# Performance work log

Hardware: AMD Instinct MI355X
Metric: run time of the kernel (lower is better)

## Reference

```python
import jax, jax.numpy as jnp
import numpy as np


def setup_inputs() -> dict:
    key = jax.random.key(0)
    ks = jax.random.split(key, 7)
    B, F, D = 1024, 32, 64
    H = [128, 128, 128]
    x = jax.random.normal(ks[0], (B, F, D), dtype=jnp.float32)
    # Conv1d(k=1) weights: (out, in) where in = prev_field * F, Kaiming-ish scale
    W0 = jax.random.normal(ks[1], (H[0], F * F), dtype=jnp.float32) * 0.02
    b0 = jnp.zeros((H[0],), dtype=jnp.float32)
    W1 = jax.random.normal(ks[2], (H[1], H[0] * F), dtype=jnp.float32) * 0.02
    b1 = jnp.zeros((H[1],), dtype=jnp.float32)
    W2 = jax.random.normal(ks[3], (H[2], H[1] * F), dtype=jnp.float32) * 0.02
    b2 = jnp.zeros((H[2],), dtype=jnp.float32)
    return {"x": x, "W0": W0, "b0": b0, "W1": W1, "b1": b1, "W2": W2, "b2": b2}


def reference(x, W0, b0, W1, b1, W2, b2):
    # CIN: per layer, outer product of current hidden with base fields along
    # embed dim, then 1x1 conv (channel mix) + ReLU. We fuse the bhmd
    # intermediate directly into the contraction: W reshaped to (o, h, m)
    # matches torch's reshape(b, h*m, d) channel ordering (h major, m minor).
    F = x.shape[1]
    x0 = x  # (b, m=F, d)
    h = x
    res = []
    for W, b in ((W0, b0), (W1, b1), (W2, b2)):
        o = W.shape[0]
        Wr = W.reshape(o, h.shape[1], F)  # (o, h, m)
        z = jnp.einsum('bhd,bmd,ohm->bod', h, x0, Wr) + b[None, :, None]
        h = jax.nn.relu(z)
        res.append(h)
    out = jnp.concatenate(res, axis=1)  # (b, sum(H), d)
    return jnp.sum(out, axis=-1)  # (b, sum(H))
```

## Files before the change

### kernel.cpp

```cpp
#include <hip/hip_runtime.h>
#include <stdint.h>


typedef __attribute__((ext_vector_type(8))) _Float16 f16x8;
typedef __attribute__((ext_vector_type(2))) _Float16 f16x2;
typedef __attribute__((ext_vector_type(4))) float f32x4;
typedef __attribute__((ext_vector_type(16))) float f32x16;
typedef __attribute__((ext_vector_type(4))) int i32x4;
typedef __attribute__((ext_vector_type(2))) int i32x2;

union AB {
  i32x4 i;
  f16x8 h;
  uint32_t u[4];
};
union AB2 {
  i32x2 i;
  uint32_t u[2];
};

static __device__ __forceinline__ uint32_t pkmul(uint32_t a, uint32_t b) {
  f16x2 r = __builtin_bit_cast(f16x2, a) * __builtin_bit_cast(f16x2, b);
  return __builtin_bit_cast(uint32_t, r);
}
static __device__ __forceinline__ uint32_t pkcvt(float a, float b) {
  return __builtin_bit_cast(uint32_t, __builtin_amdgcn_cvt_pkrtz(a, b));
}

#define HP 140

__global__ __launch_bounds__(256, 4) void cin_main(
    const float* __restrict__ x, const uint16_t* __restrict__ wp,
    const float* __restrict__ bias0, const float* __restrict__ bias1,
    const float* __restrict__ bias2, float* __restrict__ out) {
  __shared__ __align__(16) uint16_t hT[64][HP];

  const int tid = threadIdx.x;
  const int ot = tid >> 6, lane = tid & 63;
  const int hi = lane >> 5;
  const int l31 = lane & 31;
  const int b = blockIdx.x;

  for (int e = tid; e < 2048; e += 256) {
    int m = e >> 6, d = e & 63;
    hT[d][m] =
        __builtin_bit_cast(uint16_t, (_Float16)x[(size_t)b * 2048 + m * 64 + d]);
  }
  __syncthreads();

  AB xf[2][2];
#pragma unroll
  for (int dt = 0; dt < 2; ++dt)
#pragma unroll
    for (int s = 0; s < 2; ++s) {
      AB2 lo = *(const AB2*)&hT[dt * 32 + l31][s * 16 + hi * 8];
      AB2 hi4 = *(const AB2*)&hT[dt * 32 + l31][s * 16 + hi * 8 + 4];
      xf[dt][s].u[0] = lo.u[0];
      xf[dt][s].u[1] = lo.u[1];
      xf[dt][s].u[2] = hi4.u[0];
      xf[dt][s].u[3] = hi4.u[1];
    }

  f32x16 acc[2][2];

#pragma unroll
  for (int L = 0; L < 3; ++L) {
    const int Kch = (L == 0) ? 32 : 128;
    const uint16_t* wl = (L == 0) ? wp : (L == 1) ? wp + 131072 : wp + 655360;
    const float* bias = (L == 0) ? bias0 : (L == 1) ? bias1 : bias2;

    const uint16_t* wptr = wl + (size_t)ot * Kch * 1024 + lane * 8;

#pragma unroll
    for (int dt = 0; dt < 2; ++dt)
#pragma unroll
      for (int s = 0; s < 2; ++s)
#pragma unroll
        for (int r = 0; r < 16; ++r) acc[dt][s][r] = 0.f;

    AB wbuf[2][4];
    uint32_t hvA[2], hvB[2];

    auto loadSlot = [&](int sl, int c) {
      int cw = (c < Kch) ? c : 0;
#pragma unroll
      for (int cc = 0; cc < 2; ++cc)
#pragma unroll
        for (int s = 0; s < 2; ++s)
          wbuf[sl][cc * 2 + s].i =
              *(const i32x4*)(wptr + (size_t)(cw + cc) * 1024 + s * 512);
    };
    auto loadHv = [&](uint32_t (&hv)[2], int c) {
      int cw = (c < Kch) ? c : 0;
#pragma unroll
      for (int dt = 0; dt < 2; ++dt)
        hv[dt] = *(const uint32_t*)&hT[dt * 32 + l31][cw];
    };
    auto computeStep = [&](const AB (&wb)[4], const uint32_t (&hv)[2]) {
#pragma unroll
      for (int cc = 0; cc < 2; ++cc) {
        uint32_t hd0 = __builtin_amdgcn_perm(hv[0], hv[0],
                                             cc ? 0x03020302u : 0x01000100u);
        uint32_t hd1 = __builtin_amdgcn_perm(hv[1], hv[1],
                                             cc ? 0x03020302u : 0x01000100u);
#pragma unroll
        for (int s = 0; s < 2; ++s) {
          AB bf0, bf1;
#pragma unroll
          for (int k = 0; k < 4; ++k) {
            bf0.u[k] = pkmul(hd0, xf[0][s].u[k]);
            bf1.u[k] = pkmul(hd1, xf[1][s].u[k]);
          }
          acc[0][s] = __builtin_amdgcn_mfma_f32_32x32x16_f16(
              wb[cc * 2 + s].h, bf0.h, acc[0][s], 0, 0, 0);
          acc[1][s] = __builtin_amdgcn_mfma_f32_32x32x16_f16(
              wb[cc * 2 + s].h, bf1.h, acc[1][s], 0, 0, 0);
        }
      }
    };

    loadSlot(0, 0);
    loadSlot(1, 2);
    loadHv(hvA, 0);

#pragma unroll 1
    for (int c0 = 0; c0 < Kch; c0 += 4) {
      loadHv(hvB, c0 + 2);
      computeStep(wbuf[0], hvA);
      loadSlot(0, c0 + 4);
      __builtin_amdgcn_sched_barrier(0);
      loadHv(hvA, c0 + 4);
      computeStep(wbuf[1], hvB);
      loadSlot(1, c0 + 6);
      __builtin_amdgcn_sched_barrier(0);
    }

    f32x16 a0, a1;
#pragma unroll
    for (int r = 0; r < 16; ++r) {
      a0[r] = acc[0][0][r] + acc[0][1][r];
      a1[r] = acc[1][0][r] + acc[1][1][r];
    }

    f32x4 bv[4];
#pragma unroll
    for (int rg = 0; rg < 4; ++rg)
      bv[rg] = *(const f32x4*)(bias + ot * 32 + 8 * rg + 4 * hi);
#pragma unroll
    for (int r = 0; r < 16; ++r) {
      a0[r] = fmaxf(a0[r] + bv[r >> 2][r & 3], 0.f);
      a1[r] = fmaxf(a1[r] + bv[r >> 2][r & 3], 0.f);
    }

    if (L < 2) {
      __syncthreads();
#pragma unroll
      for (int rg = 0; rg < 4; ++rg) {
        uint2 pk0, pk1;
        pk0.x = pkcvt(a0[4 * rg + 0], a0[4 * rg + 1]);
        pk0.y = pkcvt(a0[4 * rg + 2], a0[4 * rg + 3]);
        pk1.x = pkcvt(a1[4 * rg + 0], a1[4 * rg + 1]);
        pk1.y = pkcvt(a1[4 * rg + 2], a1[4 * rg + 3]);
        int ch = ot * 32 + 8 * rg + 4 * hi;
        *(uint2*)&hT[l31][ch] = pk0;
        *(uint2*)&hT[32 + l31][ch] = pk1;
      }
    }

#pragma unroll
    for (int rg = 0; rg < 4; ++rg) {
      f32x4 s4;
#pragma unroll
      for (int rr = 0; rr < 4; ++rr) {
        float s = a0[4 * rg + rr] + a1[4 * rg + rr];
        s += __shfl_xor(s, 1);
        s += __shfl_xor(s, 2);
        s += __shfl_xor(s, 4);
        s += __shfl_xor(s, 8);
        s += __shfl_xor(s, 16);
        s4[rr] = s;
      }
      if (l31 == 0)
        *(f32x4*)(out + (size_t)b * 384 + L * 128 + ot * 32 + 8 * rg + 4 * hi) = s4;
    }

    if (L < 2) __syncthreads();
  }
}

__global__ void pack_w_all(const float* __restrict__ W0, const float* __restrict__ W1,
                           const float* __restrict__ W2, uint16_t* __restrict__ Wp) {
  int blk = blockIdx.x;
  const float* W;
  uint16_t* dst;
  int kshift;
  if (blk < 64)       { W = W0; dst = Wp;          kshift = 5; }
  else if (blk < 320) { W = W1; dst = Wp + 131072; kshift = 7; blk -= 64; }
  else                { W = W2; dst = Wp + 655360; kshift = 7; blk -= 320; }
  int idx = blk * 256 + threadIdx.x;
  int Kq = 1 << (kshift + 2);
  int o = idx >> (kshift + 2);
  int kq = idx & (Kq - 1);
  int c = kq >> 2, s = (kq >> 1) & 1, hi = kq & 1;
  int ot = o >> 5, li = o & 31;
  const float* src = W + ((size_t)o << (kshift + 5)) + kq * 8;
  uint4 val;
  val.x = pkcvt(src[0], src[1]);
  val.y = pkcvt(src[2], src[3]);
  val.z = pkcvt(src[4], src[5]);
  val.w = pkcvt(src[6], src[7]);
  size_t d16 = ((((size_t)(ot << kshift) + c) * 2 + s) << 9) + (hi << 8) + (li << 3);
  *(uint4*)(dst + d16) = val;
}

extern "C" void kernel_launch(void* const* d_in, const int* in_sizes, int n_in,
                              void* d_out, int out_size, void* d_ws, size_t ws_size,
                              hipStream_t stream) {
  (void)in_sizes; (void)n_in; (void)out_size; (void)ws_size;
  const float* x  = (const float*)d_in[0];
  const float* W0 = (const float*)d_in[1];
  const float* b0 = (const float*)d_in[2];
  const float* W1 = (const float*)d_in[3];
  const float* b1 = (const float*)d_in[4];
  const float* W2 = (const float*)d_in[5];
  const float* b2 = (const float*)d_in[6];
  uint16_t* wpacked = (uint16_t*)d_ws;

  hipLaunchKernelGGL(pack_w_all, dim3(576), dim3(256), 0, stream, W0, W1, W2, wpacked);
  hipLaunchKernelGGL(cin_main, dim3(1024), dim3(256), 0, stream,
                     x, wpacked, b0, b1, b2, (float*)d_out);
}
```

Measured before the change: 221.7 us.

## Process two batch rows per block to reuse weight fragments across samples

Each block now handles two batch samples, so every weight fragment loaded from global memory feeds twice as many MFMAs. The grid halves, shared memory doubles and the occupancy hint drops from 4 to 3 waves per SIMD. The loop is peeled so the last step no longer issues clamped prefetches, and the weight base address is made wave-uniform through readfirstlane. This trades higher register and LDS use, and less parallelism, for lower weight-load traffic per sample.

```diff
diff --git a/kernel.cpp b/kernel.cpp
--- a/kernel.cpp
+++ b/kernel.cpp
@@ -29,37 +29,40 @@
 
 #define HP 140
 
-__global__ __launch_bounds__(256, 4) void cin_main(
+__global__ __launch_bounds__(256, 3) void cin_main(
     const float* __restrict__ x, const uint16_t* __restrict__ wp,
     const float* __restrict__ bias0, const float* __restrict__ bias1,
     const float* __restrict__ bias2, float* __restrict__ out) {
-  __shared__ __align__(16) uint16_t hT[64][HP];
+  __shared__ __align__(16) uint16_t hT[2][64][HP];
 
   const int tid = threadIdx.x;
   const int ot = tid >> 6, lane = tid & 63;
   const int hi = lane >> 5;
   const int l31 = lane & 31;
-  const int b = blockIdx.x;
-
-  for (int e = tid; e < 2048; e += 256) {
-    int m = e >> 6, d = e & 63;
-    hT[d][m] =
-        __builtin_bit_cast(uint16_t, (_Float16)x[(size_t)b * 2048 + m * 64 + d]);
+  const int lane8 = lane * 8;
+  const int bb = blockIdx.x * 2;
+
+  for (int e = tid; e < 4096; e += 256) {
+    int p = e >> 11, m = (e >> 6) & 31, d = e & 63;
+    hT[p][d][m] =
+        __builtin_bit_cast(uint16_t, (_Float16)x[(size_t)(bb + p) * 2048 + m * 64 + d]);
   }
   __syncthreads();
 
-  AB xf[2][2];
-#pragma unroll
-  for (int dt = 0; dt < 2; ++dt)
-#pragma unroll
-    for (int s = 0; s < 2; ++s) {
-      AB2 lo = *(const AB2*)&hT[dt * 32 + l31][s * 16 + hi * 8];
-      AB2 hi4 = *(const AB2*)&hT[dt * 32 + l31][s * 16 + hi * 8 + 4];
-      xf[dt][s].u[0] = lo.u[0];
-      xf[dt][s].u[1] = lo.u[1];
-      xf[dt][s].u[2] = hi4.u[0];
-      xf[dt][s].u[3] = hi4.u[1];
-    }
+  AB xf[2][2][2];
+#pragma unroll
+  for (int b2 = 0; b2 < 2; ++b2)
+#pragma unroll
+    for (int dt = 0; dt < 2; ++dt)
+#pragma unroll
+      for (int s = 0; s < 2; ++s) {
+        AB2 lo = *(const AB2*)&hT[b2][dt * 32 + l31][s * 16 + hi * 8];
+        AB2 hi4 = *(const AB2*)&hT[b2][dt * 32 + l31][s * 16 + hi * 8 + 4];
+        xf[b2][dt][s].u[0] = lo.u[0];
+        xf[b2][dt][s].u[1] = lo.u[1];
+        xf[b2][dt][s].u[2] = hi4.u[0];
+        xf[b2][dt][s].u[3] = hi4.u[1];
+      }
 
   f32x16 acc[2][2];
 
@@ -69,53 +72,57 @@
     const uint16_t* wl = (L == 0) ? wp : (L == 1) ? wp + 131072 : wp + 655360;
     const float* bias = (L == 0) ? bias0 : (L == 1) ? bias1 : bias2;
 
-    const uint16_t* wptr = wl + (size_t)ot * Kch * 1024 + lane * 8;
-
-#pragma unroll
-    for (int dt = 0; dt < 2; ++dt)
-#pragma unroll
-      for (int s = 0; s < 2; ++s)
-#pragma unroll
-        for (int r = 0; r < 16; ++r) acc[dt][s][r] = 0.f;
-
-    AB wbuf[2][4];
-    uint32_t hvA[2], hvB[2];
+    const uint16_t* pb =
+        wl + ((size_t)__builtin_amdgcn_readfirstlane(ot * Kch) << 10);
+
+#pragma unroll
+    for (int b2 = 0; b2 < 2; ++b2)
+#pragma unroll
+      for (int dt = 0; dt < 2; ++dt)
+#pragma unroll
+        for (int r = 0; r < 16; ++r) acc[b2][dt][r] = 0.f;
+
+    AB wbuf[2][2][2];
+    uint32_t hvA[2][2], hvB[2][2];
 
     auto loadSlot = [&](int sl, int c) {
-      int cw = (c < Kch) ? c : 0;
 #pragma unroll
       for (int cc = 0; cc < 2; ++cc)
 #pragma unroll
         for (int s = 0; s < 2; ++s)
-          wbuf[sl][cc * 2 + s].i =
-              *(const i32x4*)(wptr + (size_t)(cw + cc) * 1024 + s * 512);
+          wbuf[sl][cc][s].i =
+              *(const i32x4*)(pb + ((c + cc) << 10) + (s << 9) + lane8);
     };
-    auto loadHv = [&](uint32_t (&hv)[2], int c) {
-      int cw = (c < Kch) ? c : 0;
-#pragma unroll
-      for (int dt = 0; dt < 2; ++dt)
-        hv[dt] = *(const uint32_t*)&hT[dt * 32 + l31][cw];
+    auto loadHv = [&](uint32_t (&hv)[2][2], int c) {
+#pragma unroll
+      for (int b2 = 0; b2 < 2; ++b2)
+#pragma unroll
+        for (int dt = 0; dt < 2; ++dt)
+          hv[b2][dt] = *(const uint32_t*)&hT[b2][dt * 32 + l31][c];
     };
-    auto computeStep = [&](const AB (&wb)[4], const uint32_t (&hv)[2]) {
+    auto computeStep = [&](const AB (&wb)[2][2], const uint32_t (&hv)[2][2]) {
 #pragma unroll
       for (int cc = 0; cc < 2; ++cc) {
-        uint32_t hd0 = __builtin_amdgcn_perm(hv[0], hv[0],
-                                             cc ? 0x03020302u : 0x01000100u);
-        uint32_t hd1 = __builtin_amdgcn_perm(hv[1], hv[1],
-                                             cc ? 0x03020302u : 0x01000100u);
-#pragma unroll
-        for (int s = 0; s < 2; ++s) {
-          AB bf0, bf1;
-#pragma unroll
-          for (int k = 0; k < 4; ++k) {
-            bf0.u[k] = pkmul(hd0, xf[0][s].u[k]);
-            bf1.u[k] = pkmul(hd1, xf[1][s].u[k]);
-          }
-          acc[0][s] = __builtin_amdgcn_mfma_f32_32x32x16_f16(
-              wb[cc * 2 + s].h, bf0.h, acc[0][s], 0, 0, 0);
-          acc[1][s] = __builtin_amdgcn_mfma_f32_32x32x16_f16(
-              wb[cc * 2 + s].h, bf1.h, acc[1][s], 0, 0, 0);
-        }
+        uint32_t hd[2][2];
+#pragma unroll
+        for (int b2 = 0; b2 < 2; ++b2)
+#pragma unroll
+          for (int dt = 0; dt < 2; ++dt)
+            hd[b2][dt] = __builtin_amdgcn_perm(
+                hv[b2][dt], hv[b2][dt], cc ? 0x03020302u : 0x01000100u);
+#pragma unroll
+        for (int s = 0; s < 2; ++s)
+#pragma unroll
+          for (int b2 = 0; b2 < 2; ++b2)
+#pragma unroll
+            for (int dt = 0; dt < 2; ++dt) {
+              AB bf;
+#pragma unroll
+              for (int k = 0; k < 4; ++k)
+                bf.u[k] = pkmul(hd[b2][dt], xf[b2][dt][s].u[k]);
+              acc[b2][dt] = __builtin_amdgcn_mfma_f32_32x32x16_f16(
+                  wb[cc][s].h, bf.h, acc[b2][dt], 0, 0, 0);
+            }
       }
     };
 
@@ -124,7 +131,7 @@
     loadHv(hvA, 0);
 
 #pragma unroll 1
-    for (int c0 = 0; c0 < Kch; c0 += 4) {
+    for (int c0 = 0; c0 < Kch - 4; c0 += 4) {
       loadHv(hvB, c0 + 2);
       computeStep(wbuf[0], hvA);
       loadSlot(0, c0 + 4);
@@ -134,55 +141,57 @@
       loadSlot(1, c0 + 6);
       __builtin_amdgcn_sched_barrier(0);
     }
-
-    f32x16 a0, a1;
-#pragma unroll
-    for (int r = 0; r < 16; ++r) {
-      a0[r] = acc[0][0][r] + acc[0][1][r];
-      a1[r] = acc[1][0][r] + acc[1][1][r];
-    }
-
-    f32x4 bv[4];
-#pragma unroll
-    for (int rg = 0; rg < 4; ++rg)
-      bv[rg] = *(const f32x4*)(bias + ot * 32 + 8 * rg + 4 * hi);
-#pragma unroll
-    for (int r = 0; r < 16; ++r) {
-      a0[r] = fmaxf(a0[r] + bv[r >> 2][r & 3], 0.f);
-      a1[r] = fmaxf(a1[r] + bv[r >> 2][r & 3], 0.f);
+    loadHv(hvB, Kch - 2);
+    computeStep(wbuf[0], hvA);
+    computeStep(wbuf[1], hvB);
+
+#pragma unroll
+    for (int rg = 0; rg < 4; ++rg) {
+      f32x4 bv = *(const f32x4*)(bias + ot * 32 + 8 * rg + 4 * hi);
+#pragma unroll
+      for (int b2 = 0; b2 < 2; ++b2)
+#pragma unroll
+        for (int dt = 0; dt < 2; ++dt)
+#pragma unroll
+          for (int rr = 0; rr < 4; ++rr)
+            acc[b2][dt][4 * rg + rr] =
+                fmaxf(acc[b2][dt][4 * rg + rr] + bv[rr], 0.f);
     }
 
     if (L < 2) {
       __syncthreads();
 #pragma unroll
+      for (int b2 = 0; b2 < 2; ++b2)
+#pragma unroll
+        for (int dt = 0; dt < 2; ++dt)
+#pragma unroll
+          for (int rg = 0; rg < 4; ++rg) {
+            uint2 pk;
+            pk.x = pkcvt(acc[b2][dt][4 * rg + 0], acc[b2][dt][4 * rg + 1]);
+            pk.y = pkcvt(acc[b2][dt][4 * rg + 2], acc[b2][dt][4 * rg + 3]);
+            *(uint2*)&hT[b2][dt * 32 + l31][ot * 32 + 8 * rg + 4 * hi] = pk;
+          }
+    }
+
+#pragma unroll
+    for (int b2 = 0; b2 < 2; ++b2)
+#pragma unroll
       for (int rg = 0; rg < 4; ++rg) {
-        uint2 pk0, pk1;
-        pk0.x = pkcvt(a0[4 * rg + 0], a0[4 * rg + 1]);
-        pk0.y = pkcvt(a0[4 * rg + 2], a0[4 * rg + 3]);
-        pk1.x = pkcvt(a1[4 * rg + 0], a1[4 * rg + 1]);
-        pk1.y = pkcvt(a1[4 * rg + 2], a1[4 * rg + 3]);
-        int ch = ot * 32 + 8 * rg + 4 * hi;
-        *(uint2*)&hT[l31][ch] = pk0;
-        *(uint2*)&hT[32 + l31][ch] = pk1;
+        f32x4 s4;
+#pragma unroll
+        for (int rr = 0; rr < 4; ++rr) {
+          float s = acc[b2][0][4 * rg + rr] + acc[b2][1][4 * rg + rr];
+          s += __shfl_xor(s, 1);
+          s += __shfl_xor(s, 2);
+          s += __shfl_xor(s, 4);
+          s += __shfl_xor(s, 8);
+          s += __shfl_xor(s, 16);
+          s4[rr] = s;
+        }
+        if (l31 == 0)
+          *(f32x4*)(out + (size_t)(bb + b2) * 384 + L * 128 + ot * 32 +
+                    8 * rg + 4 * hi) = s4;
       }
-    }
-
-#pragma unroll
-    for (int rg = 0; rg < 4; ++rg) {
-      f32x4 s4;
-#pragma unroll
-      for (int rr = 0; rr < 4; ++rr) {
-        float s = a0[4 * rg + rr] + a1[4 * rg + rr];
-        s += __shfl_xor(s, 1);
-        s += __shfl_xor(s, 2);
-        s += __shfl_xor(s, 4);
-        s += __shfl_xor(s, 8);
-        s += __shfl_xor(s, 16);
-        s4[rr] = s;
-      }
-      if (l31 == 0)
-        *(f32x4*)(out + (size_t)b * 384 + L * 128 + ot * 32 + 8 * rg + 4 * hi) = s4;
-    }
 
     if (L < 2) __syncthreads();
   }
@@ -227,6 +236,6 @@
   uint16_t* wpacked = (uint16_t*)d_ws;
 
   hipLaunchKernelGGL(pack_w_all, dim3(576), dim3(256), 0, stream, W0, W1, W2, wpacked);
-  hipLaunchKernelGGL(cin_main, dim3(1024), dim3(256), 0, stream,
+  hipLaunchKernelGGL(cin_main, dim3(512), dim3(256), 0, stream,
                      x, wpacked, b0, b1, b2, (float*)d_out);
 }
```

Measured after the change: 200.6 us. 1.11x faster.
